# Kernel optimization log

Hardware: AMD Instinct MI355X
Metric: run time of the kernel (lower is better)

## Reference

```python
import jax, jax.numpy as jnp
import numpy as np

D_MODEL = 512
INF = 1e9
TEMP = np.sqrt(D_MODEL).astype(np.float32)


def setup_inputs() -> dict:
    key = jax.random.key(0)
    kq, kk, kv, km = jax.random.split(key, 4)
    B, L, D = 64, 1024, 64  # B = batch*heads
    q = jax.random.normal(kq, (B, L, D), dtype=jnp.float32)
    k = jax.random.normal(kk, (B, L, D), dtype=jnp.float32)
    v = jax.random.normal(kv, (B, L, D), dtype=jnp.float32)
    attn_mask = jax.random.randint(km, (B, L, L), 0, 2).astype(jnp.bool_)
    return {"q": q, "k": k, "v": v, "attn_mask": attn_mask}


def reference(q, k, v, attn_mask):
    # scores: [b, len_q, len_k]
    attn = jnp.einsum('bqd,bkd->bqk', q, k) / TEMP
    attn = jnp.where(attn_mask, -INF, attn)
    attn = jax.nn.softmax(attn, axis=2)
    # dropout p=0.0 -> identity
    out = jnp.einsum('bqk,bkd->bqd', attn, v)
    return out
```

## Files before the change

kernel.cpp:

```cpp
#include <hip/hip_runtime.h>
#include <hip/hip_bf16.h>


typedef __attribute__((ext_vector_type(4))) float f32x4;
typedef __attribute__((ext_vector_type(8))) short bf16x8;
typedef __attribute__((ext_vector_type(4))) short short4v;

constexpr int B_ = 64;
constexpr int L_ = 1024;
constexpr int D_ = 64;
constexpr int QBLK = 64;
constexpr int KV = 64;
constexpr int NKV = L_ / KV;
constexpr int STR = 72;
constexpr float INV_TEMP = 0.04419417382415922f;
constexpr float NEG = -1e9f;

__device__ inline short f2bf(float f) {
  __hip_bfloat16 h = __float2bfloat16(f);
  short s; __builtin_memcpy(&s, &h, 2);
  return s;
}

__global__ __launch_bounds__(256) void attn_fwd(
    const float* __restrict__ Q, const float* __restrict__ K,
    const float* __restrict__ V, const int* __restrict__ M,
    float* __restrict__ O)
{
  __shared__ short k_lds[2][KV][STR];
  __shared__ short vt_lds[2][D_][STR];
  __shared__ short p_lds[4][16][STR];

  const int tid  = threadIdx.x;
  const int w    = tid >> 6;
  const int lane = tid & 63;
  const int g    = lane >> 4;
  const int c    = lane & 15;
  const int b    = blockIdx.y;
  const int q0   = blockIdx.x * QBLK;

  bf16x8 qf[2];
  {
    const float* qp = Q + ((size_t)b * L_ + q0 + w * 16 + c) * D_ + g * 8;
#pragma unroll
    for (int ks = 0; ks < 2; ++ks) {
      f32x4 x0 = *(const f32x4*)(qp + ks * 32);
      f32x4 x1 = *(const f32x4*)(qp + ks * 32 + 4);
      bf16x8 t;
      t[0] = f2bf(x0[0]); t[1] = f2bf(x0[1]); t[2] = f2bf(x0[2]); t[3] = f2bf(x0[3]);
      t[4] = f2bf(x1[0]); t[5] = f2bf(x1[1]); t[6] = f2bf(x1[2]); t[7] = f2bf(x1[3]);
      qf[ks] = t;
    }
  }

  const float* Kb = K + (size_t)b * L_ * D_;
  const float* Vb = V + (size_t)b * L_ * D_;
  const int* mlane = M + (size_t)b * L_ * L_ + (size_t)(q0 + w * 16 + c) * L_ + 4 * g;

  f32x4 kreg[4], vreg[4];
  int4  mA[4], mB[4];
  const int vkey4 = (tid & 15) * 4;
  const int vd4   = (tid >> 4) * 4;

  auto load_kv = [&](int t) {
    const float* ksrc = Kb + (size_t)(t * KV) * D_;
    const float* vsrc = Vb + (size_t)(t * KV) * D_;
#pragma unroll
    for (int i = 0; i < 4; ++i) {
      kreg[i] = *(const f32x4*)(ksrc + (size_t)(tid + i * 256) * 4);
      vreg[i] = *(const f32x4*)(vsrc + (size_t)(vkey4 + i) * D_ + vd4);
    }
  };
  auto load_m = [&](int t, int4 (&mr)[4]) {
#pragma unroll
    for (int f = 0; f < 4; ++f) mr[f] = *(const int4*)(mlane + t * KV + f * 16);
  };
  auto write_kv = [&](int buf) {
#pragma unroll
    for (int i = 0; i < 4; ++i) {
      const int idx = tid + i * 256;
      const int row = idx >> 4;
      const int d4  = (idx & 15) * 4;
      f32x4 kx = kreg[i];
      short4v ks4 = { f2bf(kx[0]), f2bf(kx[1]), f2bf(kx[2]), f2bf(kx[3]) };
      *(short4v*)&k_lds[buf][row][d4] = ks4;
      const int jj = (i + (tid >> 4)) & 3;
      short4v vt4 = { f2bf(vreg[0][jj]), f2bf(vreg[1][jj]),
                      f2bf(vreg[2][jj]), f2bf(vreg[3][jj]) };
      *(short4v*)&vt_lds[buf][vd4 + jj][vkey4] = vt4;
    }
  };

  f32x4 acc[4];
#pragma unroll
  for (int i = 0; i < 4; ++i) acc[i] = (f32x4){0.f, 0.f, 0.f, 0.f};
  float m_run = -INFINITY;
  float l_run = 0.f;

  load_kv(0);
  load_m(0, mA);
  write_kv(0);
  __syncthreads();

  auto body = [&](int t, bool has_next, int4 (&mc)[4], int4 (&mn)[4]) {
    const int cur = t & 1;
    if (has_next) { load_kv(t + 1); load_m(t + 1, mn); }

    f32x4 sc[4];
#pragma unroll
    for (int f = 0; f < 4; ++f) {
      f32x4 a = (f32x4){0.f, 0.f, 0.f, 0.f};
#pragma unroll
      for (int ks = 0; ks < 2; ++ks) {
        bf16x8 kf = *(const bf16x8*)&k_lds[cur][f * 16 + c][ks * 32 + g * 8];
        a = __builtin_amdgcn_mfma_f32_16x16x32_bf16(kf, qf[ks], a, 0, 0, 0);
      }
      sc[f] = a;
    }

#pragma unroll
    for (int f = 0; f < 4; ++f) {
      const int4 mm = mc[f];
      sc[f][0] = mm.x ? NEG : sc[f][0] * INV_TEMP;
      sc[f][1] = mm.y ? NEG : sc[f][1] * INV_TEMP;
      sc[f][2] = mm.z ? NEG : sc[f][2] * INV_TEMP;
      sc[f][3] = mm.w ? NEG : sc[f][3] * INV_TEMP;
    }

    float x = -INFINITY;
#pragma unroll
    for (int f = 0; f < 4; ++f)
#pragma unroll
      for (int r = 0; r < 4; ++r) x = fmaxf(x, sc[f][r]);
    x = fmaxf(x, __shfl_xor(x, 16, 64));
    x = fmaxf(x, __shfl_xor(x, 32, 64));
    const float m_new = fmaxf(m_run, x);
    const float alpha = __expf(m_run - m_new);
    float s = 0.f;
#pragma unroll
    for (int f = 0; f < 4; ++f)
#pragma unroll
      for (int r = 0; r < 4; ++r) {
        sc[f][r] = __expf(sc[f][r] - m_new);
        s += sc[f][r];
      }
    s += __shfl_xor(s, 16, 64);
    s += __shfl_xor(s, 32, 64);
    l_run = l_run * alpha + s;
    m_run = m_new;

    float ar[4];
#pragma unroll
    for (int r = 0; r < 4; ++r)
      ar[r] = __shfl(alpha, (lane & 48) | (g * 4 + r), 64);
#pragma unroll
    for (int fd = 0; fd < 4; ++fd)
#pragma unroll
      for (int r = 0; r < 4; ++r) acc[fd][r] *= ar[r];

#pragma unroll
    for (int f = 0; f < 4; ++f) {
      short4v pk = { f2bf(sc[f][0]), f2bf(sc[f][1]), f2bf(sc[f][2]), f2bf(sc[f][3]) };
      *(short4v*)&p_lds[w][c][f * 16 + 4 * g] = pk;
    }

#pragma unroll
    for (int ks = 0; ks < 2; ++ks) {
      bf16x8 pa = *(const bf16x8*)&p_lds[w][c][ks * 32 + g * 8];
#pragma unroll
      for (int fd = 0; fd < 4; ++fd) {
        bf16x8 vb = *(const bf16x8*)&vt_lds[cur][fd * 16 + c][ks * 32 + g * 8];
        acc[fd] = __builtin_amdgcn_mfma_f32_16x16x32_bf16(pa, vb, acc[fd], 0, 0, 0);
      }
    }

    if (has_next) write_kv(cur ^ 1);
    __syncthreads();
  };

  for (int tt = 0; tt < NKV; tt += 2) {
    body(tt,     true,          mA, mB);
    body(tt + 1, tt + 2 < NKV,  mB, mA);
  }

  const float li = 1.0f / l_run;
  float lr[4];
#pragma unroll
  for (int r = 0; r < 4; ++r)
    lr[r] = __shfl(li, (lane & 48) | (g * 4 + r), 64);
  float* orow = O + ((size_t)b * L_ + q0 + w * 16 + g * 4) * D_;
#pragma unroll
  for (int fd = 0; fd < 4; ++fd)
#pragma unroll
    for (int r = 0; r < 4; ++r)
      orow[(size_t)r * D_ + fd * 16 + c] = acc[fd][r] * lr[r];
}

extern "C" void kernel_launch(void* const* d_in, const int* in_sizes, int n_in,
                              void* d_out, int out_size, void* d_ws, size_t ws_size,
                              hipStream_t stream) {
  const float* q = (const float*)d_in[0];
  const float* k = (const float*)d_in[1];
  const float* v = (const float*)d_in[2];
  const int* m = (const int*)d_in[3];
  float* o = (float*)d_out;
  dim3 grid(L_ / QBLK, B_);
  attn_fwd<<<grid, 256, 0, stream>>>(q, k, v, m, o);
}
```

Baseline: 100.3 us.

## Keep P in registers via shuffles, lazy rescale, exp2 softmax, bit-packed mask

The P tile is now passed from the QK MFMA output layout to the PV operand layout with lane shuffles, so the p_lds shared-memory round trip goes away. The softmax folds log2(e) into the scale and uses exp2f. The running max is only updated when some row's new max exceeds the old one by more than a threshold. The row sum is kept per lane and reduced once at the end, and the mask is packed into a 16-bit register word. Launch bounds now request 4 blocks per CU, trading register headroom for occupancy and adding a wave-wide vote branch.

```diff
diff --git a/kernel.cpp b/kernel.cpp
--- a/kernel.cpp
+++ b/kernel.cpp
@@ -13,23 +13,27 @@
 constexpr int KV = 64;
 constexpr int NKV = L_ / KV;
 constexpr int STR = 72;
-constexpr float INV_TEMP = 0.04419417382415922f;
+constexpr float SC2 = 0.06376003f;
 constexpr float NEG = -1e9f;
+constexpr float THR = 8.0f;
 
 __device__ inline short f2bf(float f) {
   __hip_bfloat16 h = __float2bfloat16(f);
   short s; __builtin_memcpy(&s, &h, 2);
   return s;
 }
-
-__global__ __launch_bounds__(256) void attn_fwd(
+__device__ inline unsigned int pk2(float a, float b) {
+  return (unsigned int)(unsigned short)f2bf(a)
+       | ((unsigned int)(unsigned short)f2bf(b) << 16);
+}
+
+__global__ __launch_bounds__(256, 4) void attn_fwd(
     const float* __restrict__ Q, const float* __restrict__ K,
     const float* __restrict__ V, const int* __restrict__ M,
     float* __restrict__ O)
 {
   __shared__ short k_lds[2][KV][STR];
   __shared__ short vt_lds[2][D_][STR];
-  __shared__ short p_lds[4][16][STR];
 
   const int tid  = threadIdx.x;
   const int w    = tid >> 6;
@@ -58,7 +62,6 @@
   const int* mlane = M + (size_t)b * L_ * L_ + (size_t)(q0 + w * 16 + c) * L_ + 4 * g;
 
   f32x4 kreg[4], vreg[4];
-  int4  mA[4], mB[4];
   const int vkey4 = (tid & 15) * 4;
   const int vd4   = (tid >> 4) * 4;
 
@@ -70,10 +73,6 @@
       kreg[i] = *(const f32x4*)(ksrc + (size_t)(tid + i * 256) * 4);
       vreg[i] = *(const f32x4*)(vsrc + (size_t)(vkey4 + i) * D_ + vd4);
     }
-  };
-  auto load_m = [&](int t, int4 (&mr)[4]) {
-#pragma unroll
-    for (int f = 0; f < 4; ++f) mr[f] = *(const int4*)(mlane + t * KV + f * 16);
   };
   auto write_kv = [&](int buf) {
 #pragma unroll
@@ -90,6 +89,17 @@
       *(short4v*)&vt_lds[buf][vd4 + jj][vkey4] = vt4;
     }
   };
+  auto packm = [&](const int4* lm) {
+    unsigned int mp = 0;
+#pragma unroll
+    for (int f = 0; f < 4; ++f) {
+      mp |= (lm[f].x != 0 ? 1u : 0u) << (f * 4 + 0);
+      mp |= (lm[f].y != 0 ? 1u : 0u) << (f * 4 + 1);
+      mp |= (lm[f].z != 0 ? 1u : 0u) << (f * 4 + 2);
+      mp |= (lm[f].w != 0 ? 1u : 0u) << (f * 4 + 3);
+    }
+    return mp;
+  };
 
   f32x4 acc[4];
 #pragma unroll
@@ -97,14 +107,26 @@
   float m_run = -INFINITY;
   float l_run = 0.f;
 
-  load_kv(0);
-  load_m(0, mA);
-  write_kv(0);
+  unsigned int mcA, mcB;
+  {
+    load_kv(0);
+    int4 lm0[4];
+#pragma unroll
+    for (int f = 0; f < 4; ++f) lm0[f] = *(const int4*)(mlane + f * 16);
+    write_kv(0);
+    mcA = packm(lm0);
+  }
   __syncthreads();
 
-  auto body = [&](int t, bool has_next, int4 (&mc)[4], int4 (&mn)[4]) {
+  auto body = [&](int t, bool has_next, unsigned int mc, unsigned int& mnext) {
     const int cur = t & 1;
-    if (has_next) { load_kv(t + 1); load_m(t + 1, mn); }
+    int4 lmn[4];
+    if (has_next) {
+      load_kv(t + 1);
+#pragma unroll
+      for (int f = 0; f < 4; ++f)
+        lmn[f] = *(const int4*)(mlane + (t + 1) * KV + f * 16);
+    }
 
     f32x4 sc[4];
 #pragma unroll
@@ -119,71 +141,99 @@
     }
 
 #pragma unroll
+    for (int f = 0; f < 4; ++f)
+#pragma unroll
+      for (int r = 0; r < 4; ++r)
+        sc[f][r] = ((mc >> (f * 4 + r)) & 1u) ? NEG : sc[f][r] * SC2;
+
+    float xl = sc[0][0];
+#pragma unroll
+    for (int f = 0; f < 4; ++f)
+#pragma unroll
+      for (int r = 0; r < 4; ++r) xl = fmaxf(xl, sc[f][r]);
+    if (!__all(xl <= m_run + THR)) {
+      float x = fmaxf(xl, __shfl_xor(xl, 16, 64));
+      x = fmaxf(x, __shfl_xor(x, 32, 64));
+      const float m_new = fmaxf(m_run, x);
+      const float alpha = exp2f(m_run - m_new);
+      l_run *= alpha;
+      float ar[4];
+#pragma unroll
+      for (int r = 0; r < 4; ++r)
+        ar[r] = __shfl(alpha, (lane & 48) | (g * 4 + r), 64);
+#pragma unroll
+      for (int fd = 0; fd < 4; ++fd)
+#pragma unroll
+        for (int r = 0; r < 4; ++r) acc[fd][r] *= ar[r];
+      m_run = m_new;
+    }
+    float s = 0.f;
+#pragma unroll
+    for (int f = 0; f < 4; ++f)
+#pragma unroll
+      for (int r = 0; r < 4; ++r) {
+        const float p = exp2f(sc[f][r] - m_run);
+        sc[f][r] = p;
+        s += p;
+      }
+    l_run += s;
+
+    unsigned int pd[4][2];
+#pragma unroll
     for (int f = 0; f < 4; ++f) {
-      const int4 mm = mc[f];
-      sc[f][0] = mm.x ? NEG : sc[f][0] * INV_TEMP;
-      sc[f][1] = mm.y ? NEG : sc[f][1] * INV_TEMP;
-      sc[f][2] = mm.z ? NEG : sc[f][2] * INV_TEMP;
-      sc[f][3] = mm.w ? NEG : sc[f][3] * INV_TEMP;
-    }
-
-    float x = -INFINITY;
-#pragma unroll
-    for (int f = 0; f < 4; ++f)
-#pragma unroll
-      for (int r = 0; r < 4; ++r) x = fmaxf(x, sc[f][r]);
-    x = fmaxf(x, __shfl_xor(x, 16, 64));
-    x = fmaxf(x, __shfl_xor(x, 32, 64));
-    const float m_new = fmaxf(m_run, x);
-    const float alpha = __expf(m_run - m_new);
-    float s = 0.f;
-#pragma unroll
-    for (int f = 0; f < 4; ++f)
-#pragma unroll
-      for (int r = 0; r < 4; ++r) {
-        sc[f][r] = __expf(sc[f][r] - m_new);
-        s += sc[f][r];
+      pd[f][0] = pk2(sc[f][0], sc[f][1]);
+      pd[f][1] = pk2(sc[f][2], sc[f][3]);
+    }
+    const int rev2 = ((g & 1) << 1) | (g >> 1);
+    const int srcA = rev2 * 16 + c;
+    const int srcB = srcA ^ 16;
+    const bool podd = (g & 1) != 0;
+    const bool gh   = (g >= 2);
+    unsigned int d0[4], d1[4];
+#pragma unroll
+    for (int k = 0; k < 4; ++k) {
+      const int fb = 2 * (k >> 1);
+      const int hh = k & 1;
+      const unsigned int pubA = podd ? pd[fb + 1][hh] : pd[fb + 0][hh];
+      const unsigned int pubB = podd ? pd[fb + 0][hh] : pd[fb + 1][hh];
+      const unsigned int rvA = (unsigned int)__shfl((int)pubA, srcA, 64);
+      const unsigned int rvB = (unsigned int)__shfl((int)pubB, srcB, 64);
+      if (k < 2) {
+        if (gh) { d0[2 + hh] = rvA; d0[hh] = rvB; }
+        else    { d0[hh] = rvA; d0[2 + hh] = rvB; }
+      } else {
+        if (gh) { d1[2 + hh] = rvA; d1[hh] = rvB; }
+        else    { d1[hh] = rvA; d1[2 + hh] = rvB; }
       }
-    s += __shfl_xor(s, 16, 64);
-    s += __shfl_xor(s, 32, 64);
-    l_run = l_run * alpha + s;
-    m_run = m_new;
-
-    float ar[4];
-#pragma unroll
-    for (int r = 0; r < 4; ++r)
-      ar[r] = __shfl(alpha, (lane & 48) | (g * 4 + r), 64);
-#pragma unroll
-    for (int fd = 0; fd < 4; ++fd)
-#pragma unroll
-      for (int r = 0; r < 4; ++r) acc[fd][r] *= ar[r];
-
-#pragma unroll
-    for (int f = 0; f < 4; ++f) {
-      short4v pk = { f2bf(sc[f][0]), f2bf(sc[f][1]), f2bf(sc[f][2]), f2bf(sc[f][3]) };
-      *(short4v*)&p_lds[w][c][f * 16 + 4 * g] = pk;
-    }
-
-#pragma unroll
-    for (int ks = 0; ks < 2; ++ks) {
-      bf16x8 pa = *(const bf16x8*)&p_lds[w][c][ks * 32 + g * 8];
-#pragma unroll
-      for (int fd = 0; fd < 4; ++fd) {
-        bf16x8 vb = *(const bf16x8*)&vt_lds[cur][fd * 16 + c][ks * 32 + g * 8];
-        acc[fd] = __builtin_amdgcn_mfma_f32_16x16x32_bf16(pa, vb, acc[fd], 0, 0, 0);
-      }
-    }
-
-    if (has_next) write_kv(cur ^ 1);
+    }
+    bf16x8 pa0, pa1;
+    __builtin_memcpy(&pa0, d0, 16);
+    __builtin_memcpy(&pa1, d1, 16);
+
+#pragma unroll
+    for (int fd = 0; fd < 4; ++fd) {
+      bf16x8 vb0 = *(const bf16x8*)&vt_lds[cur][fd * 16 + c][g * 8];
+      acc[fd] = __builtin_amdgcn_mfma_f32_16x16x32_bf16(pa0, vb0, acc[fd], 0, 0, 0);
+      bf16x8 vb1 = *(const bf16x8*)&vt_lds[cur][fd * 16 + c][32 + g * 8];
+      acc[fd] = __builtin_amdgcn_mfma_f32_16x16x32_bf16(pa1, vb1, acc[fd], 0, 0, 0);
+    }
+
+    if (has_next) {
+      write_kv(cur ^ 1);
+      mnext = packm(lmn);
+    }
     __syncthreads();
   };
 
   for (int tt = 0; tt < NKV; tt += 2) {
-    body(tt,     true,          mA, mB);
-    body(tt + 1, tt + 2 < NKV,  mB, mA);
+    body(tt,     true,         mcA, mcB);
+    body(tt + 1, tt + 2 < NKV, mcB, mcA);
   }
 
-  const float li = 1.0f / l_run;
+  float l = l_run;
+  l += __shfl_xor(l, 16, 64);
+  l += __shfl_xor(l, 32, 64);
+  const float li = 1.0f / l;
   float lr[4];
 #pragma unroll
   for (int r = 0; r < 4; ++r)
```

Result: slower. 150.0 us (+49.5%).

## Split KV range across two wave groups per block and merge softmax states

Applied to the files above, without the earlier changes.

Doubles the block to 512 threads, with each half of the waves processing half of the key/value tiles for the same query block. The halves then combine their running max/sum and accumulators through shared memory. Double-buffered LDS is replaced with a single buffer per half, guarded by two barriers per tile. The aim is more in-flight memory traffic and shorter serial loops per wave, at the cost of extra barriers and a final reduction step.

```diff
diff --git a/kernel.cpp b/kernel.cpp
--- a/kernel.cpp
+++ b/kernel.cpp
@@ -11,10 +11,13 @@
 constexpr int D_ = 64;
 constexpr int QBLK = 64;
 constexpr int KV = 64;
-constexpr int NKV = L_ / KV;
+constexpr int NT_H = 8;
 constexpr int STR = 72;
 constexpr float INV_TEMP = 0.04419417382415922f;
 constexpr float NEG = -1e9f;
+
+constexpr int HBUF = 64 * STR * 2;
+constexpr int PLDS = 8 * 16 * STR * 2;
 
 __device__ inline short f2bf(float f) {
   __hip_bfloat16 h = __float2bfloat16(f);
@@ -22,26 +25,31 @@
   return s;
 }
 
-__global__ __launch_bounds__(256) void attn_fwd(
+__global__ __launch_bounds__(512, 4) void attn_fwd(
     const float* __restrict__ Q, const float* __restrict__ K,
     const float* __restrict__ V, const int* __restrict__ M,
     float* __restrict__ O)
 {
-  __shared__ short k_lds[2][KV][STR];
-  __shared__ short vt_lds[2][D_][STR];
-  __shared__ short p_lds[4][16][STR];
+  __shared__ __align__(16) unsigned char smem[4 * HBUF + PLDS + 512];
 
   const int tid  = threadIdx.x;
   const int w    = tid >> 6;
+  const int half = w >> 2;
+  const int w4   = w & 3;
   const int lane = tid & 63;
   const int g    = lane >> 4;
   const int c    = lane & 15;
+  const int htid = tid & 255;
   const int b    = blockIdx.y;
   const int q0   = blockIdx.x * QBLK;
 
+  short (*k_lds)[STR]  = (short(*)[STR])(smem + half * 2 * HBUF);
+  short (*vt_lds)[STR] = (short(*)[STR])(smem + half * 2 * HBUF + HBUF);
+  short (*p_lds)[STR]  = (short(*)[STR])(smem + 4 * HBUF + w * 16 * STR * 2);
+
   bf16x8 qf[2];
   {
-    const float* qp = Q + ((size_t)b * L_ + q0 + w * 16 + c) * D_ + g * 8;
+    const float* qp = Q + ((size_t)b * L_ + q0 + w4 * 16 + c) * D_ + g * 8;
 #pragma unroll
     for (int ks = 0; ks < 2; ++ks) {
       f32x4 x0 = *(const f32x4*)(qp + ks * 32);
@@ -53,41 +61,42 @@
     }
   }
 
-  const float* Kb = K + (size_t)b * L_ * D_;
-  const float* Vb = V + (size_t)b * L_ * D_;
-  const int* mlane = M + (size_t)b * L_ * L_ + (size_t)(q0 + w * 16 + c) * L_ + 4 * g;
+  const float* Kb = K + (size_t)b * L_ * D_ + (size_t)half * NT_H * KV * D_;
+  const float* Vb = V + (size_t)b * L_ * D_ + (size_t)half * NT_H * KV * D_;
+  const int* mlane = M + (size_t)b * L_ * L_
+                   + (size_t)(q0 + w4 * 16 + c) * L_ + half * (NT_H * KV) + 4 * g;
+
+  const int vkey4 = (htid & 15) * 4;
+  const int vd4   = (htid >> 4) * 4;
 
   f32x4 kreg[4], vreg[4];
   int4  mA[4], mB[4];
-  const int vkey4 = (tid & 15) * 4;
-  const int vd4   = (tid >> 4) * 4;
 
   auto load_kv = [&](int t) {
     const float* ksrc = Kb + (size_t)(t * KV) * D_;
     const float* vsrc = Vb + (size_t)(t * KV) * D_;
 #pragma unroll
     for (int i = 0; i < 4; ++i) {
-      kreg[i] = *(const f32x4*)(ksrc + (size_t)(tid + i * 256) * 4);
+      kreg[i] = *(const f32x4*)(ksrc + (size_t)(htid + i * 256) * 4);
       vreg[i] = *(const f32x4*)(vsrc + (size_t)(vkey4 + i) * D_ + vd4);
     }
   };
   auto load_m = [&](int t, int4 (&mr)[4]) {
 #pragma unroll
-    for (int f = 0; f < 4; ++f) mr[f] = *(const int4*)(mlane + t * KV + f * 16);
-  };
-  auto write_kv = [&](int buf) {
+    for (int f = 0; f < 4; ++f)
+      mr[f] = *(const int4*)(mlane + t * KV + f * 16);
+  };
+  auto write_kv = [&]() {
 #pragma unroll
     for (int i = 0; i < 4; ++i) {
-      const int idx = tid + i * 256;
-      const int row = idx >> 4;
-      const int d4  = (idx & 15) * 4;
-      f32x4 kx = kreg[i];
-      short4v ks4 = { f2bf(kx[0]), f2bf(kx[1]), f2bf(kx[2]), f2bf(kx[3]) };
-      *(short4v*)&k_lds[buf][row][d4] = ks4;
-      const int jj = (i + (tid >> 4)) & 3;
+      const int idx = htid + i * 256;
+      short4v ks4 = { f2bf(kreg[i][0]), f2bf(kreg[i][1]),
+                      f2bf(kreg[i][2]), f2bf(kreg[i][3]) };
+      *(short4v*)&k_lds[idx >> 4][(idx & 15) * 4] = ks4;
+      const int jj = (i + (htid >> 4)) & 3;
       short4v vt4 = { f2bf(vreg[0][jj]), f2bf(vreg[1][jj]),
                       f2bf(vreg[2][jj]), f2bf(vreg[3][jj]) };
-      *(short4v*)&vt_lds[buf][vd4 + jj][vkey4] = vt4;
+      *(short4v*)&vt_lds[vd4 + jj][vkey4] = vt4;
     }
   };
 
@@ -99,11 +108,10 @@
 
   load_kv(0);
   load_m(0, mA);
-  write_kv(0);
+  write_kv();
   __syncthreads();
 
-  auto body = [&](int t, bool has_next, int4 (&mc)[4], int4 (&mn)[4]) {
-    const int cur = t & 1;
+  auto body = [&](int t, int4 (&mc)[4], int4 (&mn)[4], bool has_next) {
     if (has_next) { load_kv(t + 1); load_m(t + 1, mn); }
 
     f32x4 sc[4];
@@ -112,7 +120,7 @@
       f32x4 a = (f32x4){0.f, 0.f, 0.f, 0.f};
 #pragma unroll
       for (int ks = 0; ks < 2; ++ks) {
-        bf16x8 kf = *(const bf16x8*)&k_lds[cur][f * 16 + c][ks * 32 + g * 8];
+        bf16x8 kf = *(const bf16x8*)&k_lds[f * 16 + c][ks * 32 + g * 8];
         a = __builtin_amdgcn_mfma_f32_16x16x32_bf16(kf, qf[ks], a, 0, 0, 0);
       }
       sc[f] = a;
@@ -127,7 +135,7 @@
       sc[f][3] = mm.w ? NEG : sc[f][3] * INV_TEMP;
     }
 
-    float x = -INFINITY;
+    float x = sc[0][0];
 #pragma unroll
     for (int f = 0; f < 4; ++f)
 #pragma unroll
@@ -160,40 +168,67 @@
 
 #pragma unroll
     for (int f = 0; f < 4; ++f) {
-      short4v pk = { f2bf(sc[f][0]), f2bf(sc[f][1]), f2bf(sc[f][2]), f2bf(sc[f][3]) };
-      *(short4v*)&p_lds[w][c][f * 16 + 4 * g] = pk;
+      short4v pk = { f2bf(sc[f][0]), f2bf(sc[f][1]),
+                     f2bf(sc[f][2]), f2bf(sc[f][3]) };
+      *(short4v*)&p_lds[c][f * 16 + 4 * g] = pk;
     }
 
 #pragma unroll
     for (int ks = 0; ks < 2; ++ks) {
-      bf16x8 pa = *(const bf16x8*)&p_lds[w][c][ks * 32 + g * 8];
+      bf16x8 pa = *(const bf16x8*)&p_lds[c][ks * 32 + g * 8];
 #pragma unroll
       for (int fd = 0; fd < 4; ++fd) {
-        bf16x8 vb = *(const bf16x8*)&vt_lds[cur][fd * 16 + c][ks * 32 + g * 8];
+        bf16x8 vb = *(const bf16x8*)&vt_lds[fd * 16 + c][ks * 32 + g * 8];
         acc[fd] = __builtin_amdgcn_mfma_f32_16x16x32_bf16(pa, vb, acc[fd], 0, 0, 0);
       }
     }
 
-    if (has_next) write_kv(cur ^ 1);
-    __syncthreads();
-  };
-
-  for (int tt = 0; tt < NKV; tt += 2) {
-    body(tt,     true,          mA, mB);
-    body(tt + 1, tt + 2 < NKV,  mB, mA);
-  }
-
-  const float li = 1.0f / l_run;
-  float lr[4];
-#pragma unroll
-  for (int r = 0; r < 4; ++r)
-    lr[r] = __shfl(li, (lane & 48) | (g * 4 + r), 64);
-  float* orow = O + ((size_t)b * L_ + q0 + w * 16 + g * 4) * D_;
-#pragma unroll
-  for (int fd = 0; fd < 4; ++fd)
-#pragma unroll
-    for (int r = 0; r < 4; ++r)
-      orow[(size_t)r * D_ + fd * 16 + c] = acc[fd][r] * lr[r];
+    if (has_next) {
+      __syncthreads();
+      write_kv();
+      __syncthreads();
+    }
+  };
+
+  for (int tt = 0; tt < NT_H; tt += 2) {
+    body(tt,     mA, mB, true);
+    body(tt + 1, mB, mA, tt + 2 < NT_H);
+  }
+
+  __syncthreads();
+  f32x4* cacc = (f32x4*)smem;
+  float2* cml = (float2*)(smem + 4 * HBUF + PLDS);
+  if (half == 1) {
+#pragma unroll
+    for (int fd = 0; fd < 4; ++fd)
+      cacc[(w4 * 64 + lane) * 4 + fd] = acc[fd];
+    if (g == 0) cml[w4 * 16 + c] = make_float2(m_run, l_run);
+  }
+  __syncthreads();
+  if (half == 0) {
+    const float2 mlB = cml[w4 * 16 + c];
+    const float Mx = fmaxf(m_run, mlB.x);
+    const float wA = __expf(m_run - Mx);
+    const float wB = __expf(mlB.x - Mx);
+    const float li = 1.0f / (wA * l_run + wB * mlB.y);
+    float arA[4], arB[4], lr[4];
+#pragma unroll
+    for (int r = 0; r < 4; ++r) {
+      const int src = (lane & 48) | (g * 4 + r);
+      arA[r] = __shfl(wA, src, 64);
+      arB[r] = __shfl(wB, src, 64);
+      lr[r]  = __shfl(li, src, 64);
+    }
+    float* orow = O + ((size_t)b * L_ + q0 + w4 * 16 + g * 4) * D_;
+#pragma unroll
+    for (int fd = 0; fd < 4; ++fd) {
+      const f32x4 ab = cacc[(w4 * 64 + lane) * 4 + fd];
+#pragma unroll
+      for (int r = 0; r < 4; ++r)
+        orow[(size_t)r * D_ + fd * 16 + c] =
+            (arA[r] * acc[fd][r] + arB[r] * ab[r]) * lr[r];
+    }
+  }
 }
 
 extern "C" void kernel_launch(void* const* d_in, const int* in_sizes, int n_in,
@@ -205,5 +240,5 @@
   const int* m = (const int*)d_in[3];
   float* o = (float*)d_out;
   dim3 grid(L_ / QBLK, B_);
-  attn_fwd<<<grid, 256, 0, stream>>>(q, k, v, m, o);
+  attn_fwd<<<grid, 512, 0, stream>>>(q, k, v, m, o);
 }
```

Result: slower. 232.2 us (+131.5%).

## Prefetch mask two tiles ahead, remap blocks per XCD, raise occupancy hint

Applied to the files above, without the earlier changes.

The mask prefetch is now two KV tiles deep: the current tile's mask is copied out of the buffer, which is then refilled for tile t+2, and a sched_barrier keeps the loads issued ahead of compute. Blocks are remapped onto a 1D grid so that all query blocks of one batch land on the same XCD, improving L2 reuse of K and V. launch_bounds now asks for 3 blocks per CU, which limits registers per thread. The extra prefetch depth hides more of the mask-load latency but holds more registers live and risks spills.

```diff
diff --git a/kernel.cpp b/kernel.cpp
--- a/kernel.cpp
+++ b/kernel.cpp
@@ -22,7 +22,7 @@
   return s;
 }
 
-__global__ __launch_bounds__(256) void attn_fwd(
+__global__ __launch_bounds__(256, 3) void attn_fwd(
     const float* __restrict__ Q, const float* __restrict__ K,
     const float* __restrict__ V, const int* __restrict__ M,
     float* __restrict__ O)
@@ -36,8 +36,12 @@
   const int lane = tid & 63;
   const int g    = lane >> 4;
   const int c    = lane & 15;
-  const int b    = blockIdx.y;
-  const int q0   = blockIdx.x * QBLK;
+
+  const int p   = blockIdx.x;
+  const int xcd = p & 7;
+  const int j   = p >> 3;
+  const int b   = xcd + 8 * (j >> 4);
+  const int q0  = (j & 15) * QBLK;
 
   bf16x8 qf[2];
   {
@@ -79,11 +83,9 @@
 #pragma unroll
     for (int i = 0; i < 4; ++i) {
       const int idx = tid + i * 256;
-      const int row = idx >> 4;
-      const int d4  = (idx & 15) * 4;
-      f32x4 kx = kreg[i];
-      short4v ks4 = { f2bf(kx[0]), f2bf(kx[1]), f2bf(kx[2]), f2bf(kx[3]) };
-      *(short4v*)&k_lds[buf][row][d4] = ks4;
+      short4v ks4 = { f2bf(kreg[i][0]), f2bf(kreg[i][1]),
+                      f2bf(kreg[i][2]), f2bf(kreg[i][3]) };
+      *(short4v*)&k_lds[buf][idx >> 4][(idx & 15) * 4] = ks4;
       const int jj = (i + (tid >> 4)) & 3;
       short4v vt4 = { f2bf(vreg[0][jj]), f2bf(vreg[1][jj]),
                       f2bf(vreg[2][jj]), f2bf(vreg[3][jj]) };
@@ -98,13 +100,20 @@
   float l_run = 0.f;
 
   load_kv(0);
+  write_kv(0);
   load_m(0, mA);
-  write_kv(0);
+  load_m(1, mB);
   __syncthreads();
 
-  auto body = [&](int t, bool has_next, int4 (&mc)[4], int4 (&mn)[4]) {
+  auto body = [&](int t, int4 (&mbuf)[4], bool refill) {
     const int cur = t & 1;
-    if (has_next) { load_kv(t + 1); load_m(t + 1, mn); }
+    const bool has_next = (t + 1 < NKV);
+    if (has_next) load_kv(t + 1);
+    int4 mc[4];
+#pragma unroll
+    for (int f = 0; f < 4; ++f) mc[f] = mbuf[f];
+    if (refill) load_m(t + 2, mbuf);
+    __builtin_amdgcn_sched_barrier(0);
 
     f32x4 sc[4];
 #pragma unroll
@@ -127,7 +136,7 @@
       sc[f][3] = mm.w ? NEG : sc[f][3] * INV_TEMP;
     }
 
-    float x = -INFINITY;
+    float x = sc[0][0];
 #pragma unroll
     for (int f = 0; f < 4; ++f)
 #pragma unroll
@@ -160,7 +169,8 @@
 
 #pragma unroll
     for (int f = 0; f < 4; ++f) {
-      short4v pk = { f2bf(sc[f][0]), f2bf(sc[f][1]), f2bf(sc[f][2]), f2bf(sc[f][3]) };
+      short4v pk = { f2bf(sc[f][0]), f2bf(sc[f][1]),
+                     f2bf(sc[f][2]), f2bf(sc[f][3]) };
       *(short4v*)&p_lds[w][c][f * 16 + 4 * g] = pk;
     }
 
@@ -179,8 +189,8 @@
   };
 
   for (int tt = 0; tt < NKV; tt += 2) {
-    body(tt,     true,          mA, mB);
-    body(tt + 1, tt + 2 < NKV,  mB, mA);
+    body(tt,     mA, tt + 2 < NKV);
+    body(tt + 1, mB, tt + 3 < NKV);
   }
 
   const float li = 1.0f / l_run;
@@ -204,6 +214,5 @@
   const float* v = (const float*)d_in[2];
   const int* m = (const int*)d_in[3];
   float* o = (float*)d_out;
-  dim3 grid(L_ / QBLK, B_);
-  attn_fwd<<<grid, 256, 0, stream>>>(q, k, v, m, o);
+  attn_fwd<<<dim3(1024), 256, 0, stream>>>(q, k, v, m, o);
 }
```

New measurement: 97.46 us (median of 3 runs). 2.9% less time.
